# Performance work log

Measured on AMD Instinct MI355X. Metric: run time of the kernel, lower is better.

## Reference

```python
import jax, jax.numpy as jnp
import numpy as np
from jax import lax

K = 3       # kernel_size
STRIDE = 1
PAD = 1
DIL = 1


def setup_inputs() -> dict:
    key = jax.random.key(0)
    ks = jax.random.split(key, 4)
    B, Cin, Cout, H, W = 4, 128, 256, 64, 64
    x = jax.random.normal(ks[0], (B, Cin, H, W), jnp.float32)
    # offset/mask conv params: out channels = 3*K*K (groups=1). Small weights
    # keep predicted offsets within a few pixels (module inits them to zero).
    om_w = jax.random.normal(ks[1], (3 * K * K, Cin, K, K), jnp.float32) * 0.01
    om_b = jnp.zeros((3 * K * K,), jnp.float32)
    weight = jax.random.normal(ks[2], (Cout, Cin, K, K), jnp.float32) * (1.0 / np.sqrt(Cin * K * K))
    bias = jnp.zeros((Cout,), jnp.float32)
    return {"x": x, "om_w": om_w, "om_b": om_b, "weight": weight, "bias": bias}


def _deform_conv(x, om_w, om_b, weight, bias):
    B, Cin, H, W = x.shape
    Cout = weight.shape[0]
    kk = K * K

    # offset/mask conv (stride/pad/dilation same as main conv)
    om = lax.conv_general_dilated(
        x, om_w, (STRIDE, STRIDE), [(PAD, PAD), (PAD, PAD)],
        rhs_dilation=(DIL, DIL), dimension_numbers=('NCHW', 'OIHW', 'NCHW'))
    om = om + om_b[None, :, None, None]
    Ho, Wo = om.shape[2], om.shape[3]

    off = om[:, :2 * kk].reshape(B, 2, kk, Ho, Wo)
    off_x, off_y = off[:, 0], off[:, 1]           # [B,kk,Ho,Wo]
    mask = jax.nn.sigmoid(om[:, 2 * kk:])          # [B,kk,Ho,Wo]

    # base grid (output pixel -> input pixel of kernel center)
    gy, gx = jnp.meshgrid(jnp.arange(Ho, dtype=x.dtype), jnp.arange(Wo, dtype=x.dtype), indexing='ij')
    base_x = gx * STRIDE - PAD
    base_y = gy * STRIDE - PAD
    # kernel taps centered at 0: arange(-(K-1)//2, (K+1)//2)
    r = jnp.arange(-(K - 1) // 2, (K + 1) // 2, dtype=x.dtype)
    koy, kox = jnp.meshgrid(r * DIL, r * DIL, indexing='ij')
    kox = kox.reshape(kk, 1, 1)
    koy = koy.reshape(kk, 1, 1)

    sx = base_x[None, None] + kox[None] + off_x    # [B,kk,Ho,Wo]
    sy = base_y[None, None] + koy[None] + off_y

    # Faithful to original: coords normalized with align_corners=True formula
    # (2*s/(size-1)-1) but grid_sample called with align_corners=False, i.e.
    # pixel coord = ((g+1)*size - 1)/2  =>  s*size/(size-1) - 0.5
    ix = sx * (W / (W - 1.0)) - 0.5
    iy = sy * (H / (H - 1.0)) - 0.5

    x0 = jnp.floor(ix)
    y0 = jnp.floor(iy)
    x1 = x0 + 1.0
    y1 = y0 + 1.0
    wx1 = ix - x0
    wx0 = 1.0 - wx1
    wy1 = iy - y0
    wy0 = 1.0 - wy1

    img = x.reshape(B, Cin, H * W)

    def gather(yy, xx):
        yi = yy.astype(jnp.int32)
        xi = xx.astype(jnp.int32)
        valid = ((yi >= 0) & (yi < H) & (xi >= 0) & (xi < W)).astype(x.dtype)
        idx = jnp.clip(yi, 0, H - 1) * W + jnp.clip(xi, 0, W - 1)   # [B,kk,Ho,Wo]
        v = jax.vmap(lambda im, i: im[:, i])(img, idx.reshape(B, -1))  # [B,Cin,kk*Ho*Wo]
        return v.reshape(B, Cin, kk, Ho, Wo) * valid[:, None]

    # bilinear (zeros padding) sample at kk taps per output pixel
    sampled = (gather(y0, x0) * (wy0 * wx0)[:, None]
               + gather(y0, x1) * (wy0 * wx1)[:, None]
               + gather(y1, x0) * (wy1 * wx0)[:, None]
               + gather(y1, x1) * (wy1 * wx1)[:, None])   # [B,Cin,kk,Ho,Wo]

    sampled = sampled * mask[:, None]
    w = weight.reshape(Cout, Cin, kk)
    out = jnp.einsum('bckhw,ock->bohw', sampled, w)
    return out + bias[None, :, None, None]


def reference(x, om_w, om_b, weight, bias):
    return _deform_conv(x, om_w, om_b, weight, bias)
```

## Files before the change

kernel.cpp:

```cpp
#include <hip/hip_runtime.h>
#include <hip/hip_bf16.h>

typedef _Float16 h4 __attribute__((ext_vector_type(4)));
typedef _Float16 h8 __attribute__((ext_vector_type(8)));
typedef float f32x4 __attribute__((ext_vector_type(4)));

#define CIN 128
#define COUT 256
#define KDIM (CIN*9)

__global__ __launch_bounds__(256) void k_pt(const float* __restrict__ x,
                                            const float* __restrict__ wgt,
                                            const float* __restrict__ om_w,
                                            unsigned short* __restrict__ xT,
                                            unsigned short* __restrict__ Wf,
                                            unsigned short* __restrict__ omWf) {
    __shared__ unsigned short tile[64][132];
    const int bid = blockIdx.x;
    if (bid < 256) {
        const int b = bid >> 6, y = bid & 63;
        const float* xp = x + (size_t)b * CIN * 4096 + y * 64;
        const int w = threadIdx.x & 63, cg = threadIdx.x >> 6;
#pragma unroll
        for (int cc = 0; cc < CIN; cc += 4) {
            int c = cc + cg;
            _Float16 hv = (_Float16)xp[(size_t)c * 4096 + w];
            tile[w][c] = *(unsigned short*)&hv;
        }
        __syncthreads();
        unsigned short* orow = xT + (size_t)(b * 4096 + y * 64) * CIN;
#pragma unroll
        for (int i = 0; i < 8; ++i) {
            int j = threadIdx.x + i * 256;
            int w2 = j >> 5, c2 = (j & 31) * 4;
            ushort4 v = *(ushort4*)&tile[w2][c2];
            ((ushort4*)orow)[j] = v;
        }
    } else if (bid < 1408) {
        int g = (bid - 256) * 256 + threadIdx.x;
        int o = g / KDIM, rem = g - o * KDIM;
        int c = rem / 9, k = rem - c * 9;
        int kc = k * 128 + c;
        int kch = kc >> 5, j = kc & 31;
        int l = ((j >> 3) << 4) | (o & 15);
        int e = j & 7, of = o >> 4;
        int f = ((kch * 16 + of) * 64 + l) * 8 + e;
        _Float16 hv = (_Float16)wgt[g];
        Wf[f] = *(unsigned short*)&hv;
    } else {
        int f = (bid - 1408) * 256 + threadIdx.x;
        int e = f & 7, l = (f >> 3) & 63, of = (f >> 9) & 1, kch = f >> 10;
        int o = of * 16 + (l & 15);
        int c = (kch & 3) * 32 + (l >> 4) * 8 + e;
        int k = kch >> 2;
        float v = (o < 27) ? om_w[(size_t)o * KDIM + c * 9 + k] : 0.f;
        _Float16 hv = (_Float16)v;
        omWf[f] = *(unsigned short*)&hv;
    }
}

__global__ __launch_bounds__(1024, 4) void k_fused(const unsigned short* __restrict__ xT_u,
                                                   const unsigned short* __restrict__ omWf_u,
                                                   const float* __restrict__ om_b,
                                                   const unsigned short* __restrict__ Wf_u,
                                                   const float* __restrict__ bias,
                                                   float* __restrict__ out) {
    const int bid = blockIdx.x;
    const int h = bid & 63, b = bid >> 6;
    const int tid = threadIdx.x;
    const int wv = tid >> 6, lane = tid & 63;
    const int khalf = lane >> 4, lr = lane & 15;

    __shared__ int   s_off[4][576];
    __shared__ float s_wt[4][576];
    __shared__ h8    s_tile[2][64 * 16];
    __shared__ float red[4][64][28];

    const _Float16* xb = (const _Float16*)xT_u + (size_t)b * (4096 * CIN);

    {
        const h8* Af = (const h8*)omWf_u;
        const int pg = wv & 3, tg = wv >> 2;
        const int pl = pg * 16 + lr;
        const int k0 = (tg == 0) ? 0 : 2 * tg + 1;
        const int k1 = (tg == 0) ? 3 : k0 + 2;
        f32x4 acc0 = (f32x4){0.f, 0.f, 0.f, 0.f};
        f32x4 acc1 = (f32x4){0.f, 0.f, 0.f, 0.f};
        for (int k = k0; k < k1; ++k) {
            const int ky = k / 3, kx = k - ky * 3;
            const int y = h + ky - 1, xq = pl + kx - 1;
            const bool valid = ((unsigned)y < 64u) && ((unsigned)xq < 64u);
            const _Float16* src = xb + ((y * 64 + xq) * CIN);
#pragma unroll
            for (int cg = 0; cg < 4; ++cg) {
                h8 bf = {};
                if (valid) bf = *(const h8*)(src + cg * 32 + khalf * 8);
                const int kch = k * 4 + cg;
                h8 a0 = Af[(kch * 2 + 0) * 64 + lane];
                h8 a1 = Af[(kch * 2 + 1) * 64 + lane];
                acc0 = __builtin_amdgcn_mfma_f32_16x16x32_f16(a0, bf, acc0, 0, 0, 0);
                acc1 = __builtin_amdgcn_mfma_f32_16x16x32_f16(a1, bf, acc1, 0, 0, 0);
            }
        }
#pragma unroll
        for (int r = 0; r < 4; ++r) {
            red[tg][pl][khalf * 4 + r] = acc0[r];
            int row1 = 16 + khalf * 4 + r;
            if (row1 < 27) red[tg][pl][row1] = acc1[r];
        }
    }
    __syncthreads();

    for (int e = tid; e < 576; e += 1024) {
        int k = e >> 6, p = e & 63;
        float offx = red[0][p][k]      + red[1][p][k]      + red[2][p][k]      + red[3][p][k]      + om_b[k];
        float offy = red[0][p][9 + k]  + red[1][p][9 + k]  + red[2][p][9 + k]  + red[3][p][9 + k]  + om_b[9 + k];
        float mv   = red[0][p][18 + k] + red[1][p][18 + k] + red[2][p][18 + k] + red[3][p][18 + k] + om_b[18 + k];
        float mask = 1.f / (1.f + __expf(-mv));
        int ky = k / 3, kx = k - ky * 3;
        const float SC = 64.f / 63.f;
        float ix = ((float)(p + kx - 2) + offx) * SC - 0.5f;
        float iy = ((float)(h + ky - 2) + offy) * SC - 0.5f;
        float fx0 = floorf(ix), fy0 = floorf(iy);
        float wx1 = ix - fx0, wx0 = 1.f - wx1;
        float wy1 = iy - fy0, wy0 = 1.f - wy1;
        int x0 = (int)fx0, y0 = (int)fy0;
        int x1 = x0 + 1, y1 = y0 + 1;
        bool vx0 = (unsigned)x0 < 64u, vx1 = (unsigned)x1 < 64u;
        bool vy0 = (unsigned)y0 < 64u, vy1 = (unsigned)y1 < 64u;
        int xc0 = min(max(x0, 0), 63), xc1 = min(max(x1, 0), 63);
        int yc0 = min(max(y0, 0), 63), yc1 = min(max(y1, 0), 63);
        s_off[0][e] = (yc0 * 64 + xc0) * CIN;
        s_off[1][e] = (yc0 * 64 + xc1) * CIN;
        s_off[2][e] = (yc1 * 64 + xc0) * CIN;
        s_off[3][e] = (yc1 * 64 + xc1) * CIN;
        s_wt[0][e] = (vy0 && vx0) ? wy0 * wx0 * mask : 0.f;
        s_wt[1][e] = (vy0 && vx1) ? wy0 * wx1 * mask : 0.f;
        s_wt[2][e] = (vy1 && vx0) ? wy1 * wx0 * mask : 0.f;
        s_wt[3][e] = (vy1 && vx1) ? wy1 * wx1 * mask : 0.f;
    }
    __syncthreads();

    const int p  = tid >> 4;
    const int ci = tid & 15;
    const h8* Wf8 = (const h8*)Wf_u;
    const int wslot = ci ^ (p & 7);

    f32x4 acc[4];
#pragma unroll
    for (int j = 0; j < 4; ++j) acc[j] = (f32x4){0.f, 0.f, 0.f, 0.f};

    {
        const int e0 = p;
        const int cb = ci * 8;
        h8 v0 = *(const h8*)(xb + s_off[0][e0] + cb);
        h8 v1 = *(const h8*)(xb + s_off[1][e0] + cb);
        h8 v2 = *(const h8*)(xb + s_off[2][e0] + cb);
        h8 v3 = *(const h8*)(xb + s_off[3][e0] + cb);
        const float m0 = s_wt[0][e0], m1 = s_wt[1][e0], m2 = s_wt[2][e0], m3 = s_wt[3][e0];
        h8 pk;
#pragma unroll
        for (int j = 0; j < 8; ++j) {
            float r = m0 * (float)v0[j] + m1 * (float)v1[j]
                    + m2 * (float)v2[j] + m3 * (float)v3[j];
            pk[j] = (_Float16)r;
        }
        s_tile[0][p * 16 + wslot] = pk;
    }
    __syncthreads();

    for (int tap = 0; tap < 9; ++tap) {
        const int cur = tap & 1;
        const int nxt = tap + 1;

        h8 v0, v1, v2, v3;
        float m0, m1, m2, m3;
        if (nxt < 9) {
            const int e = nxt * 64 + p;
            const int cb = ci * 8;
            v0 = *(const h8*)(xb + s_off[0][e] + cb);
            v1 = *(const h8*)(xb + s_off[1][e] + cb);
            v2 = *(const h8*)(xb + s_off[2][e] + cb);
            v3 = *(const h8*)(xb + s_off[3][e] + cb);
            m0 = s_wt[0][e]; m1 = s_wt[1][e]; m2 = s_wt[2][e]; m3 = s_wt[3][e];
        }

#pragma unroll
        for (int ks = 0; ks < 4; ++ks) {
            const int kch = tap * 4 + ks;
            h8 a0 = Wf8[(kch * 16 + wv) * 64 + lane];
#pragma unroll
            for (int pf = 0; pf < 4; ++pf) {
                const int row = pf * 16 + lr;
                const int slot = (ks * 4 + khalf) ^ (row & 7);
                h8 bf = s_tile[cur][row * 16 + slot];
                acc[pf] = __builtin_amdgcn_mfma_f32_16x16x32_f16(a0, bf, acc[pf], 0, 0, 0);
            }
        }

        if (nxt < 9) {
            h8 pk;
#pragma unroll
            for (int j = 0; j < 8; ++j) {
                float r = m0 * (float)v0[j] + m1 * (float)v1[j]
                        + m2 * (float)v2[j] + m3 * (float)v3[j];
                pk[j] = (_Float16)r;
            }
            s_tile[cur ^ 1][p * 16 + wslot] = pk;
        }
        __syncthreads();
    }

    float* outb = out + (size_t)b * COUT * 4096 + h * 64;
#pragma unroll
    for (int r = 0; r < 4; ++r) {
        const int o = wv * 16 + khalf * 4 + r;
        const float bo = bias[o];
        float* orow = outb + (size_t)o * 4096;
#pragma unroll
        for (int pf = 0; pf < 4; ++pf)
            orow[pf * 16 + lr] = acc[pf][r] + bo;
    }
}

extern "C" void kernel_launch(void* const* d_in, const int* in_sizes, int n_in,
                              void* d_out, int out_size, void* d_ws, size_t ws_size,
                              hipStream_t stream) {
    const float* x    = (const float*)d_in[0];
    const float* om_w = (const float*)d_in[1];
    const float* om_b = (const float*)d_in[2];
    const float* wgt  = (const float*)d_in[3];
    const float* bias = (const float*)d_in[4];
    float* out = (float*)d_out;

    char* ws = (char*)d_ws;
    unsigned short* xT   = (unsigned short*)ws;
    unsigned short* Wf   = (unsigned short*)(ws + 4194304);
    unsigned short* omWf = (unsigned short*)(ws + 4194304 + 589824);

    k_pt   <<<1552, 256, 0, stream>>>(x, wgt, om_w, xT, Wf, omWf);
    k_fused<<<256, 1024, 0, stream>>>(xT, omWf, om_b, Wf, bias, out);
}
```

Before: 40.17 us.

## Split block into dedicated MFMA waves and dedicated gather waves

The main kernel's 16 waves are now split by role instead of all doing both jobs. Eight waves run only the MFMA loop, each covering 32 output channels with two accumulator sets so each B fragment read from shared memory is used twice. The other eight waves only do the bilinear gather and fill the double-buffered shared tile for the next tap, with matched barrier counts on both sides. The aim is to overlap gather memory latency with matrix work and cut redundant LDS reads, at the cost of halving the number of waves issuing MFMAs and giving each consumer wave higher register pressure.

Result: no change. 40.07 us (-0.3%).

```diff
diff --git a/kernel.cpp b/kernel.cpp
--- a/kernel.cpp
+++ b/kernel.cpp
@@ -141,85 +141,105 @@
     }
     __syncthreads();
 
-    const int p  = tid >> 4;
-    const int ci = tid & 15;
     const h8* Wf8 = (const h8*)Wf_u;
-    const int wslot = ci ^ (p & 7);
-
-    f32x4 acc[4];
-#pragma unroll
-    for (int j = 0; j < 4; ++j) acc[j] = (f32x4){0.f, 0.f, 0.f, 0.f};
-
-    {
-        const int e0 = p;
-        const int cb = ci * 8;
-        h8 v0 = *(const h8*)(xb + s_off[0][e0] + cb);
-        h8 v1 = *(const h8*)(xb + s_off[1][e0] + cb);
-        h8 v2 = *(const h8*)(xb + s_off[2][e0] + cb);
-        h8 v3 = *(const h8*)(xb + s_off[3][e0] + cb);
-        const float m0 = s_wt[0][e0], m1 = s_wt[1][e0], m2 = s_wt[2][e0], m3 = s_wt[3][e0];
-        h8 pk;
-#pragma unroll
-        for (int j = 0; j < 8; ++j) {
-            float r = m0 * (float)v0[j] + m1 * (float)v1[j]
-                    + m2 * (float)v2[j] + m3 * (float)v3[j];
-            pk[j] = (_Float16)r;
-        }
-        s_tile[0][p * 16 + wslot] = pk;
-    }
-    __syncthreads();
-
-    for (int tap = 0; tap < 9; ++tap) {
-        const int cur = tap & 1;
-        const int nxt = tap + 1;
-
-        h8 v0, v1, v2, v3;
-        float m0, m1, m2, m3;
-        if (nxt < 9) {
-            const int e = nxt * 64 + p;
-            const int cb = ci * 8;
-            v0 = *(const h8*)(xb + s_off[0][e] + cb);
-            v1 = *(const h8*)(xb + s_off[1][e] + cb);
-            v2 = *(const h8*)(xb + s_off[2][e] + cb);
-            v3 = *(const h8*)(xb + s_off[3][e] + cb);
-            m0 = s_wt[0][e]; m1 = s_wt[1][e]; m2 = s_wt[2][e]; m3 = s_wt[3][e];
-        }
-
-#pragma unroll
-        for (int ks = 0; ks < 4; ++ks) {
-            const int kch = tap * 4 + ks;
-            h8 a0 = Wf8[(kch * 16 + wv) * 64 + lane];
-#pragma unroll
-            for (int pf = 0; pf < 4; ++pf) {
-                const int row = pf * 16 + lr;
-                const int slot = (ks * 4 + khalf) ^ (row & 7);
-                h8 bf = s_tile[cur][row * 16 + slot];
-                acc[pf] = __builtin_amdgcn_mfma_f32_16x16x32_f16(a0, bf, acc[pf], 0, 0, 0);
-            }
-        }
-
-        if (nxt < 9) {
-            h8 pk;
-#pragma unroll
-            for (int j = 0; j < 8; ++j) {
-                float r = m0 * (float)v0[j] + m1 * (float)v1[j]
-                        + m2 * (float)v2[j] + m3 * (float)v3[j];
-                pk[j] = (_Float16)r;
-            }
-            s_tile[cur ^ 1][p * 16 + wslot] = pk;
-        }
+
+    if (wv < 8) {
+        f32x4 acc[2][4];
+#pragma unroll
+        for (int i = 0; i < 2; ++i)
+#pragma unroll
+            for (int j = 0; j < 4; ++j) acc[i][j] = (f32x4){0.f, 0.f, 0.f, 0.f};
+
         __syncthreads();
-    }
-
-    float* outb = out + (size_t)b * COUT * 4096 + h * 64;
-#pragma unroll
-    for (int r = 0; r < 4; ++r) {
-        const int o = wv * 16 + khalf * 4 + r;
-        const float bo = bias[o];
-        float* orow = outb + (size_t)o * 4096;
-#pragma unroll
-        for (int pf = 0; pf < 4; ++pf)
-            orow[pf * 16 + lr] = acc[pf][r] + bo;
+
+        for (int tap = 0; tap < 9; ++tap) {
+            const int cur = tap & 1;
+#pragma unroll
+            for (int ks = 0; ks < 4; ++ks) {
+                const int kch = tap * 4 + ks;
+                h8 a0 = Wf8[(kch * 16 + wv * 2 + 0) * 64 + lane];
+                h8 a1 = Wf8[(kch * 16 + wv * 2 + 1) * 64 + lane];
+#pragma unroll
+                for (int pf = 0; pf < 4; ++pf) {
+                    const int row = pf * 16 + lr;
+                    const int slot = (ks * 4 + khalf) ^ (row & 7);
+                    h8 bf = s_tile[cur][row * 16 + slot];
+                    acc[0][pf] = __builtin_amdgcn_mfma_f32_16x16x32_f16(a0, bf, acc[0][pf], 0, 0, 0);
+                    acc[1][pf] = __builtin_amdgcn_mfma_f32_16x16x32_f16(a1, bf, acc[1][pf], 0, 0, 0);
+                }
+            }
+            __syncthreads();
+        }
+
+        float* outb = out + (size_t)b * COUT * 4096 + h * 64;
+#pragma unroll
+        for (int i = 0; i < 2; ++i) {
+#pragma unroll
+            for (int r = 0; r < 4; ++r) {
+                const int o = wv * 32 + i * 16 + khalf * 4 + r;
+                const float bo = bias[o];
+                float* orow = outb + (size_t)o * 4096;
+#pragma unroll
+                for (int pf = 0; pf < 4; ++pf)
+                    orow[pf * 16 + lr] = acc[i][pf][r] + bo;
+            }
+        }
+    } else {
+        const int t = tid - 512;
+        const int p = t >> 3;
+        const int ci2 = t & 7;
+
+        {
+            const int e0 = p;
+            const int o0 = s_off[0][e0], o1 = s_off[1][e0], o2 = s_off[2][e0], o3 = s_off[3][e0];
+            const float m0 = s_wt[0][e0], m1 = s_wt[1][e0], m2 = s_wt[2][e0], m3 = s_wt[3][e0];
+#pragma unroll
+            for (int s = 0; s < 2; ++s) {
+                const int cs = ci2 + s * 8;
+                const int cb = cs * 8;
+                h8 v0 = *(const h8*)(xb + o0 + cb);
+                h8 v1 = *(const h8*)(xb + o1 + cb);
+                h8 v2 = *(const h8*)(xb + o2 + cb);
+                h8 v3 = *(const h8*)(xb + o3 + cb);
+                h8 pk;
+#pragma unroll
+                for (int j = 0; j < 8; ++j) {
+                    float r = m0 * (float)v0[j] + m1 * (float)v1[j]
+                            + m2 * (float)v2[j] + m3 * (float)v3[j];
+                    pk[j] = (_Float16)r;
+                }
+                s_tile[0][p * 16 + (cs ^ (p & 7))] = pk;
+            }
+        }
+        __syncthreads();
+
+        for (int tap = 0; tap < 9; ++tap) {
+            const int nxt = tap + 1;
+            if (nxt < 9) {
+                const int e = nxt * 64 + p;
+                const int o0 = s_off[0][e], o1 = s_off[1][e], o2 = s_off[2][e], o3 = s_off[3][e];
+                const float m0 = s_wt[0][e], m1 = s_wt[1][e], m2 = s_wt[2][e], m3 = s_wt[3][e];
+                const int buf = nxt & 1;
+#pragma unroll
+                for (int s = 0; s < 2; ++s) {
+                    const int cs = ci2 + s * 8;
+                    const int cb = cs * 8;
+                    h8 v0 = *(const h8*)(xb + o0 + cb);
+                    h8 v1 = *(const h8*)(xb + o1 + cb);
+                    h8 v2 = *(const h8*)(xb + o2 + cb);
+                    h8 v3 = *(const h8*)(xb + o3 + cb);
+                    h8 pk;
+#pragma unroll
+                    for (int j = 0; j < 8; ++j) {
+                        float r = m0 * (float)v0[j] + m1 * (float)v1[j]
+                                + m2 * (float)v2[j] + m3 * (float)v3[j];
+                        pk[j] = (_Float16)r;
+                    }
+                    s_tile[buf][p * 16 + (cs ^ (p & 7))] = pk;
+                }
+            }
+            __syncthreads();
+        }
     }
 }
 
```
